# Performance work log

Measured on AMD Instinct MI355X. Metric: run time of the kernel, lower is better.

## Reference

```python
import jax, jax.numpy as jnp
import numpy as np

H = 1024          # hidden_size
V = 50257         # output_size (vocab)
L = 64            # max_length


def setup_inputs() -> dict:
    key = jax.random.key(0)
    ks = jax.random.split(key, 20)
    s = 0.02
    inp = {
        "input": jax.random.randint(ks[0], (1,), 0, V, dtype=jnp.int64) if jax.config.jax_enable_x64 else jax.random.randint(ks[0], (1,), 0, V, dtype=jnp.int32),
        "hidden": jax.random.normal(ks[1], (2, 1, H), dtype=jnp.float32),
        "encoder_output": jax.random.normal(ks[2], (1, 2 * H), dtype=jnp.float32),
        "encoder_outputs": jax.random.normal(ks[3], (L, 2 * H), dtype=jnp.float32),
        # parameters
        "emb": jax.random.normal(ks[4], (V, H), dtype=jnp.float32) * s,
        "attn_W": jax.random.normal(ks[5], (L, 3 * H), dtype=jnp.float32) * s,
        "attn_b": jnp.zeros((L,), dtype=jnp.float32),
        "comb_W": jax.random.normal(ks[6], (H, 3 * H), dtype=jnp.float32) * s,
        "comb_b": jnp.zeros((H,), dtype=jnp.float32),
        "Wih_f": jax.random.normal(ks[7], (3 * H, H), dtype=jnp.float32) * s,
        "Whh_f": jax.random.normal(ks[8], (3 * H, H), dtype=jnp.float32) * s,
        "bih_f": jnp.zeros((3 * H,), dtype=jnp.float32),
        "bhh_f": jnp.zeros((3 * H,), dtype=jnp.float32),
        "Wih_b": jax.random.normal(ks[9], (3 * H, H), dtype=jnp.float32) * s,
        "Whh_b": jax.random.normal(ks[10], (3 * H, H), dtype=jnp.float32) * s,
        "bih_b": jnp.zeros((3 * H,), dtype=jnp.float32),
        "bhh_b": jnp.zeros((3 * H,), dtype=jnp.float32),
        "out_W": jax.random.normal(ks[11], (V, 2 * H), dtype=jnp.float32) * s,
        "out_b": jnp.zeros((V,), dtype=jnp.float32),
    }
    return inp


def _gru_cell(x, h, Wih, Whh, bih, bhh):
    # PyTorch GRUCell gate math; x, h: (1, H)
    gi = x @ Wih.T + bih                      # (1, 3H)
    gh = h @ Whh.T + bhh                      # (1, 3H)
    ir, iz, inn = jnp.split(gi, 3, axis=1)
    hr, hz, hn = jnp.split(gh, 3, axis=1)
    r = jax.nn.sigmoid(ir + hr)
    z = jax.nn.sigmoid(iz + hz)
    n = jnp.tanh(inn + r * hn)
    return (1.0 - z) * n + z * h


def reference(input, hidden, encoder_output, encoder_outputs,
              emb, attn_W, attn_b, comb_W, comb_b,
              Wih_f, Whh_f, bih_f, bhh_f,
              Wih_b, Whh_b, bih_b, bhh_b,
              out_W, out_b):
    embedded = emb[input]                     # (1, H); dropout is identity in eval
    h0, h1 = hidden[0], hidden[1]             # (1, H) each
    cat3 = jnp.concatenate([embedded, h0, h1], axis=1)          # (1, 3H)
    attn_weights = jax.nn.softmax(cat3 @ attn_W.T + attn_b, axis=1)  # (1, L)
    attn_applied = attn_weights @ encoder_outputs               # (1, 2H)
    comb = jnp.concatenate([embedded, attn_applied], axis=1)    # (1, 3H)
    x = jax.nn.relu(comb @ comb_W.T + comb_b)                   # (1, H)
    hf = _gru_cell(x, h0, Wih_f, Whh_f, bih_f, bhh_f)           # forward dir
    hb = _gru_cell(x, h1, Wih_b, Whh_b, bih_b, bhh_b)           # backward dir (seq_len=1)
    gru_out = jnp.concatenate([hf, hb], axis=1)                 # (1, 2H)
    new_hidden = jnp.stack([hf, hb], axis=0)                    # (2, 1, H)
    log_probs = jax.nn.log_softmax(gru_out @ out_W.T + out_b, axis=1)  # (1, V)
    return (log_probs, new_hidden, attn_weights)
```

## Files before the change

kernel.cpp:

```cpp
#include <hip/hip_runtime.h>
#include <hip/hip_bf16.h>
#include <math.h>

#define H   1024
#define V   50257
#define L   64
#define H2  2048
#define H3  3072

#define WS_ATTN_LOGITS 0
#define WS_ATTNW       64
#define WS_AA          128
#define WS_X           2176
#define WS_GRU         3200
#define WS_LOGITS      5248
#define WS_RED         55552
#define WS_C           55680

__device__ inline float waveReduceSum(float v) {
#pragma unroll
    for (int off = 32; off > 0; off >>= 1) v += __shfl_down(v, off, 64);
    return v;
}
__device__ inline float waveAllMax(float v) {
#pragma unroll
    for (int off = 32; off > 0; off >>= 1) v = fmaxf(v, __shfl_xor(v, off, 64));
    return v;
}
__device__ inline float waveAllSum(float v) {
#pragma unroll
    for (int off = 32; off > 0; off >>= 1) v += __shfl_xor(v, off, 64);
    return v;
}

__global__ __launch_bounds__(256) void k_attn_logits(
        const int* __restrict__ tok_p, const float* __restrict__ hidden,
        const float* __restrict__ emb, const float* __restrict__ attn_W,
        const float* __restrict__ attn_b, float* __restrict__ ws) {
    int b = blockIdx.x;
    int tid = threadIdx.x;
    int tok = tok_p[0];
    const float4* w4   = (const float4*)(attn_W + (size_t)b * H3);
    const float4* emb4 = (const float4*)(emb + (size_t)tok * H);
    const float4* hid4 = (const float4*)hidden;
    float acc = 0.f;
#pragma unroll
    for (int k = 0; k < 3; ++k) {
        int idx = tid + k * 256;
        float4 c = (idx < 256) ? emb4[idx] : hid4[idx - 256];
        float4 w = w4[idx];
        acc += c.x * w.x + c.y * w.y + c.z * w.z + c.w * w.w;
    }
    __shared__ float red[4];
    float p = waveReduceSum(acc);
    int lane = tid & 63, wid = tid >> 6;
    if (lane == 0) red[wid] = p;
    __syncthreads();
    if (tid == 0) ws[WS_ATTN_LOGITS + b] = red[0] + red[1] + red[2] + red[3] + attn_b[b];
}

__global__ __launch_bounds__(64) void k_softmax64(float* __restrict__ ws,
                                                  float* __restrict__ d_out) {
    int lane = threadIdx.x;
    float x = ws[WS_ATTN_LOGITS + lane];
    float m = waveAllMax(x);
    float e = expf(x - m);
    float s = waveAllSum(e);
    float w = e / s;
    ws[WS_ATTNW + lane] = w;
    d_out[V + H2 + lane] = w;
}

__global__ __launch_bounds__(256) void k_attn_applied(
        const float* __restrict__ eo, float* __restrict__ ws) {
    int j = blockIdx.x * 256 + threadIdx.x;
    float acc = 0.f;
#pragma unroll 8
    for (int l = 0; l < L; ++l) acc += ws[WS_ATTNW + l] * eo[l * H2 + j];
    ws[WS_AA + j] = acc;
}

__global__ __launch_bounds__(256) void k_comb_relu(
        const int* __restrict__ tok_p, const float* __restrict__ emb,
        const float* __restrict__ comb_W, const float* __restrict__ comb_b,
        float* __restrict__ ws) {
    int tid = threadIdx.x;
    int lane = tid & 63, wid = tid >> 6;
    int r = blockIdx.x * 4 + wid;
    int tok = tok_p[0];
    const float4* emb4 = (const float4*)(emb + (size_t)tok * H);
    const float4* aa4  = (const float4*)(ws + WS_AA);
    const float4* w4   = (const float4*)(comb_W + (size_t)r * H3);
    float acc = 0.f;
#pragma unroll
    for (int k = 0; k < 12; ++k) {
        int idx = lane + k * 64;
        float4 c = (idx < 256) ? emb4[idx] : aa4[idx - 256];
        float4 w = w4[idx];
        acc += c.x * w.x + c.y * w.y + c.z * w.z + c.w * w.w;
    }
    acc = waveReduceSum(acc);
    if (lane == 0) ws[WS_X + r] = fmaxf(acc + comb_b[r], 0.f);
}

__global__ __launch_bounds__(256) void k_gru(
        const float* __restrict__ hidden,
        const float* __restrict__ Wih_f, const float* __restrict__ Whh_f,
        const float* __restrict__ bih_f, const float* __restrict__ bhh_f,
        const float* __restrict__ Wih_b, const float* __restrict__ Whh_b,
        const float* __restrict__ bih_b, const float* __restrict__ bhh_b,
        float* __restrict__ d_out, float* __restrict__ ws) {
    int tid = threadIdx.x;
    int lane = tid & 63, wid = tid >> 6;
    int w = blockIdx.x * 4 + wid;
    int dir = w >> 10;
    int i = w & (H - 1);
    const float* Wih = dir ? Wih_b : Wih_f;
    const float* Whh = dir ? Whh_b : Whh_f;
    const float* bih = dir ? bih_b : bih_f;
    const float* bhh = dir ? bhh_b : bhh_f;
    const float* h = hidden + dir * H;
    const float4* x4  = (const float4*)(ws + WS_X);
    const float4* h4  = (const float4*)h;
    const float4* wi0 = (const float4*)(Wih + (size_t)i * H);
    const float4* wi1 = (const float4*)(Wih + (size_t)(H + i) * H);
    const float4* wi2 = (const float4*)(Wih + (size_t)(2 * H + i) * H);
    const float4* wh0 = (const float4*)(Whh + (size_t)i * H);
    const float4* wh1 = (const float4*)(Whh + (size_t)(H + i) * H);
    const float4* wh2 = (const float4*)(Whh + (size_t)(2 * H + i) * H);
    float a0 = 0, a1 = 0, a2 = 0, b0 = 0, b1 = 0, b2 = 0;
#pragma unroll
    for (int k = 0; k < 4; ++k) {
        int idx = lane + k * 64;
        float4 xv = x4[idx], hv = h4[idx];
        float4 u0 = wi0[idx], u1 = wi1[idx], u2 = wi2[idx];
        float4 v0 = wh0[idx], v1 = wh1[idx], v2 = wh2[idx];
        a0 += xv.x*u0.x + xv.y*u0.y + xv.z*u0.z + xv.w*u0.w;
        a1 += xv.x*u1.x + xv.y*u1.y + xv.z*u1.z + xv.w*u1.w;
        a2 += xv.x*u2.x + xv.y*u2.y + xv.z*u2.z + xv.w*u2.w;
        b0 += hv.x*v0.x + hv.y*v0.y + hv.z*v0.z + hv.w*v0.w;
        b1 += hv.x*v1.x + hv.y*v1.y + hv.z*v1.z + hv.w*v1.w;
        b2 += hv.x*v2.x + hv.y*v2.y + hv.z*v2.z + hv.w*v2.w;
    }
    a0 = waveReduceSum(a0); a1 = waveReduceSum(a1); a2 = waveReduceSum(a2);
    b0 = waveReduceSum(b0); b1 = waveReduceSum(b1); b2 = waveReduceSum(b2);
    if (lane == 0) {
        float ir = a0 + bih[i],     iz = a1 + bih[H + i], in_ = a2 + bih[2 * H + i];
        float hr = b0 + bhh[i],     hz = b1 + bhh[H + i], hn  = b2 + bhh[2 * H + i];
        float r = 1.f / (1.f + expf(-(ir + hr)));
        float z = 1.f / (1.f + expf(-(iz + hz)));
        float n = tanhf(in_ + r * hn);
        float hv = (1.f - z) * n + z * h[i];
        d_out[V + dir * H + i] = hv;
        ws[WS_GRU + dir * H + i] = hv;
    }
}

__global__ __launch_bounds__(256) void k_out_gemv(
        const float* __restrict__ out_W, const float* __restrict__ out_b,
        float* __restrict__ ws) {
    int tid = threadIdx.x;
    int lane = tid & 63, wid = tid >> 6;
    int v = blockIdx.x * 4 + wid;
    if (v >= V) return;
    const float4* g4 = (const float4*)(ws + WS_GRU);
    const float4* w4 = (const float4*)(out_W + (size_t)v * H2);
    float acc = 0.f;
#pragma unroll
    for (int k = 0; k < 8; ++k) {
        int idx = lane + k * 64;
        float4 g = g4[idx], w = w4[idx];
        acc += g.x * w.x + g.y * w.y + g.z * w.z + g.w * w.w;
    }
    acc = waveReduceSum(acc);
    if (lane == 0) ws[WS_LOGITS + v] = acc + out_b[v];
}

__device__ inline void lse_combine(float& m, float& s, float m2, float s2) {
    float M = fmaxf(m, m2);
    s = s * expf(m - M) + s2 * expf(m2 - M);
    m = M;
}

__global__ __launch_bounds__(256) void k_lse_partial(float* __restrict__ ws) {
    int tid = blockIdx.x * 256 + threadIdx.x;
    int stride = gridDim.x * 256;
    float m = -3.0e38f, s = 0.f;
    for (int v = tid; v < V; v += stride) {
        float x = ws[WS_LOGITS + v];
        float M = fmaxf(m, x);
        s = s * expf(m - M) + expf(x - M);
        m = M;
    }
#pragma unroll
    for (int off = 32; off > 0; off >>= 1) {
        float m2 = __shfl_xor(m, off, 64);
        float s2 = __shfl_xor(s, off, 64);
        lse_combine(m, s, m2, s2);
    }
    __shared__ float mm[4], ss[4];
    int lane = threadIdx.x & 63, wid = threadIdx.x >> 6;
    if (lane == 0) { mm[wid] = m; ss[wid] = s; }
    __syncthreads();
    if (threadIdx.x == 0) {
        float M = mm[0], S = ss[0];
        lse_combine(M, S, mm[1], ss[1]);
        lse_combine(M, S, mm[2], ss[2]);
        lse_combine(M, S, mm[3], ss[3]);
        ws[WS_RED + 2 * blockIdx.x]     = M;
        ws[WS_RED + 2 * blockIdx.x + 1] = S;
    }
}

__global__ __launch_bounds__(64) void k_lse_final(float* __restrict__ ws) {
    int lane = threadIdx.x;
    float m = ws[WS_RED + 2 * lane];
    float s = ws[WS_RED + 2 * lane + 1];
#pragma unroll
    for (int off = 32; off > 0; off >>= 1) {
        float m2 = __shfl_xor(m, off, 64);
        float s2 = __shfl_xor(s, off, 64);
        lse_combine(m, s, m2, s2);
    }
    if (lane == 0) ws[WS_C] = m + logf(s);
}

__global__ __launch_bounds__(256) void k_sub(const float* __restrict__ ws,
                                             float* __restrict__ d_out) {
    int v = blockIdx.x * 256 + threadIdx.x;
    if (v < V) d_out[v] = ws[WS_LOGITS + v] - ws[WS_C];
}

extern "C" void kernel_launch(void* const* d_in, const int* in_sizes, int n_in,
                              void* d_out, int out_size, void* d_ws, size_t ws_size,
                              hipStream_t stream) {
    const int*   tok     = (const int*)  d_in[0];
    const float* hidden  = (const float*)d_in[1];
    const float* enc_outs= (const float*)d_in[3];
    const float* emb     = (const float*)d_in[4];
    const float* attn_W  = (const float*)d_in[5];
    const float* attn_b  = (const float*)d_in[6];
    const float* comb_W  = (const float*)d_in[7];
    const float* comb_b  = (const float*)d_in[8];
    const float* Wih_f   = (const float*)d_in[9];
    const float* Whh_f   = (const float*)d_in[10];
    const float* bih_f   = (const float*)d_in[11];
    const float* bhh_f   = (const float*)d_in[12];
    const float* Wih_b   = (const float*)d_in[13];
    const float* Whh_b   = (const float*)d_in[14];
    const float* bih_b   = (const float*)d_in[15];
    const float* bhh_b   = (const float*)d_in[16];
    const float* out_W   = (const float*)d_in[17];
    const float* out_b   = (const float*)d_in[18];
    float* out = (float*)d_out;
    float* ws  = (float*)d_ws;

    hipLaunchKernelGGL(k_attn_logits, dim3(64), dim3(256), 0, stream,
                       tok, hidden, emb, attn_W, attn_b, ws);
    hipLaunchKernelGGL(k_softmax64, dim3(1), dim3(64), 0, stream, ws, out);
    hipLaunchKernelGGL(k_attn_applied, dim3(8), dim3(256), 0, stream, enc_outs, ws);
    hipLaunchKernelGGL(k_comb_relu, dim3(256), dim3(256), 0, stream,
                       tok, emb, comb_W, comb_b, ws);
    hipLaunchKernelGGL(k_gru, dim3(512), dim3(256), 0, stream,
                       hidden, Wih_f, Whh_f, bih_f, bhh_f,
                       Wih_b, Whh_b, bih_b, bhh_b, out, ws);
    hipLaunchKernelGGL(k_out_gemv, dim3((V + 3) / 4), dim3(256), 0, stream,
                       out_W, out_b, ws);
    hipLaunchKernelGGL(k_lse_partial, dim3(64), dim3(256), 0, stream, ws);
    hipLaunchKernelGGL(k_lse_final, dim3(1), dim3(64), 0, stream, ws);
    hipLaunchKernelGGL(k_sub, dim3(197), dim3(256), 0, stream, ws, out);
}
```

Measured before the change: 105.7 us.

## Fuse front stages into cooperative kernel and fold LSE into output GEMV

The attention, softmax, attention-apply, combine and GRU stages are merged into one cooperative kernel with grid-wide syncs, replacing five launches. The vocab GEMV becomes a persistent grid-stride kernel that also computes per-block online log-sum-exp partials. The final reduction and subtraction are merged, so nine launches drop to three. Grid syncs cost something, and the cooperative launch needs all 512 blocks co-resident. Every block of the subtract kernel also redundantly re-reduces 1024 partials.

```diff
diff --git a/kernel.cpp b/kernel.cpp
--- a/kernel.cpp
+++ b/kernel.cpp
@@ -1,6 +1,9 @@
 #include <hip/hip_runtime.h>
 #include <hip/hip_bf16.h>
+#include <hip/hip_cooperative_groups.h>
 #include <math.h>
+
+namespace cg = cooperative_groups;
 
 #define H   1024
 #define V   50257
@@ -9,13 +12,14 @@
 #define H3  3072
 
 #define WS_ATTN_LOGITS 0
-#define WS_ATTNW       64
 #define WS_AA          128
 #define WS_X           2176
 #define WS_GRU         3200
 #define WS_LOGITS      5248
 #define WS_RED         55552
-#define WS_C           55680
+
+#define GEMV_BLOCKS 1024
+#define GEMV_WAVES  (GEMV_BLOCKS * 4)
 
 __device__ inline float waveReduceSum(float v) {
 #pragma unroll
@@ -32,177 +36,163 @@
     for (int off = 32; off > 0; off >>= 1) v += __shfl_xor(v, off, 64);
     return v;
 }
-
-__global__ __launch_bounds__(256) void k_attn_logits(
+__device__ inline void lse_combine(float& m, float& s, float m2, float s2) {
+    float M = fmaxf(m, m2);
+    s = s * expf(m - M) + s2 * expf(m2 - M);
+    m = M;
+}
+
+__global__ __launch_bounds__(256) void k_front(
         const int* __restrict__ tok_p, const float* __restrict__ hidden,
         const float* __restrict__ emb, const float* __restrict__ attn_W,
-        const float* __restrict__ attn_b, float* __restrict__ ws) {
-    int b = blockIdx.x;
-    int tid = threadIdx.x;
-    int tok = tok_p[0];
-    const float4* w4   = (const float4*)(attn_W + (size_t)b * H3);
-    const float4* emb4 = (const float4*)(emb + (size_t)tok * H);
-    const float4* hid4 = (const float4*)hidden;
-    float acc = 0.f;
-#pragma unroll
-    for (int k = 0; k < 3; ++k) {
-        int idx = tid + k * 256;
-        float4 c = (idx < 256) ? emb4[idx] : hid4[idx - 256];
-        float4 w = w4[idx];
-        acc += c.x * w.x + c.y * w.y + c.z * w.z + c.w * w.w;
-    }
-    __shared__ float red[4];
-    float p = waveReduceSum(acc);
-    int lane = tid & 63, wid = tid >> 6;
-    if (lane == 0) red[wid] = p;
-    __syncthreads();
-    if (tid == 0) ws[WS_ATTN_LOGITS + b] = red[0] + red[1] + red[2] + red[3] + attn_b[b];
-}
-
-__global__ __launch_bounds__(64) void k_softmax64(float* __restrict__ ws,
-                                                  float* __restrict__ d_out) {
-    int lane = threadIdx.x;
-    float x = ws[WS_ATTN_LOGITS + lane];
-    float m = waveAllMax(x);
-    float e = expf(x - m);
-    float s = waveAllSum(e);
-    float w = e / s;
-    ws[WS_ATTNW + lane] = w;
-    d_out[V + H2 + lane] = w;
-}
-
-__global__ __launch_bounds__(256) void k_attn_applied(
-        const float* __restrict__ eo, float* __restrict__ ws) {
-    int j = blockIdx.x * 256 + threadIdx.x;
-    float acc = 0.f;
-#pragma unroll 8
-    for (int l = 0; l < L; ++l) acc += ws[WS_ATTNW + l] * eo[l * H2 + j];
-    ws[WS_AA + j] = acc;
-}
-
-__global__ __launch_bounds__(256) void k_comb_relu(
-        const int* __restrict__ tok_p, const float* __restrict__ emb,
+        const float* __restrict__ attn_b, const float* __restrict__ eo,
         const float* __restrict__ comb_W, const float* __restrict__ comb_b,
-        float* __restrict__ ws) {
-    int tid = threadIdx.x;
-    int lane = tid & 63, wid = tid >> 6;
-    int r = blockIdx.x * 4 + wid;
-    int tok = tok_p[0];
-    const float4* emb4 = (const float4*)(emb + (size_t)tok * H);
-    const float4* aa4  = (const float4*)(ws + WS_AA);
-    const float4* w4   = (const float4*)(comb_W + (size_t)r * H3);
-    float acc = 0.f;
-#pragma unroll
-    for (int k = 0; k < 12; ++k) {
-        int idx = lane + k * 64;
-        float4 c = (idx < 256) ? emb4[idx] : aa4[idx - 256];
-        float4 w = w4[idx];
-        acc += c.x * w.x + c.y * w.y + c.z * w.z + c.w * w.w;
-    }
-    acc = waveReduceSum(acc);
-    if (lane == 0) ws[WS_X + r] = fmaxf(acc + comb_b[r], 0.f);
-}
-
-__global__ __launch_bounds__(256) void k_gru(
-        const float* __restrict__ hidden,
         const float* __restrict__ Wih_f, const float* __restrict__ Whh_f,
         const float* __restrict__ bih_f, const float* __restrict__ bhh_f,
         const float* __restrict__ Wih_b, const float* __restrict__ Whh_b,
         const float* __restrict__ bih_b, const float* __restrict__ bhh_b,
         float* __restrict__ d_out, float* __restrict__ ws) {
+    cg::grid_group grid = cg::this_grid();
     int tid = threadIdx.x;
     int lane = tid & 63, wid = tid >> 6;
-    int w = blockIdx.x * 4 + wid;
-    int dir = w >> 10;
-    int i = w & (H - 1);
-    const float* Wih = dir ? Wih_b : Wih_f;
-    const float* Whh = dir ? Whh_b : Whh_f;
-    const float* bih = dir ? bih_b : bih_f;
-    const float* bhh = dir ? bhh_b : bhh_f;
-    const float* h = hidden + dir * H;
-    const float4* x4  = (const float4*)(ws + WS_X);
-    const float4* h4  = (const float4*)h;
-    const float4* wi0 = (const float4*)(Wih + (size_t)i * H);
-    const float4* wi1 = (const float4*)(Wih + (size_t)(H + i) * H);
-    const float4* wi2 = (const float4*)(Wih + (size_t)(2 * H + i) * H);
-    const float4* wh0 = (const float4*)(Whh + (size_t)i * H);
-    const float4* wh1 = (const float4*)(Whh + (size_t)(H + i) * H);
-    const float4* wh2 = (const float4*)(Whh + (size_t)(2 * H + i) * H);
-    float a0 = 0, a1 = 0, a2 = 0, b0 = 0, b1 = 0, b2 = 0;
-#pragma unroll
-    for (int k = 0; k < 4; ++k) {
-        int idx = lane + k * 64;
-        float4 xv = x4[idx], hv = h4[idx];
-        float4 u0 = wi0[idx], u1 = wi1[idx], u2 = wi2[idx];
-        float4 v0 = wh0[idx], v1 = wh1[idx], v2 = wh2[idx];
-        a0 += xv.x*u0.x + xv.y*u0.y + xv.z*u0.z + xv.w*u0.w;
-        a1 += xv.x*u1.x + xv.y*u1.y + xv.z*u1.z + xv.w*u1.w;
-        a2 += xv.x*u2.x + xv.y*u2.y + xv.z*u2.z + xv.w*u2.w;
-        b0 += hv.x*v0.x + hv.y*v0.y + hv.z*v0.z + hv.w*v0.w;
-        b1 += hv.x*v1.x + hv.y*v1.y + hv.z*v1.z + hv.w*v1.w;
-        b2 += hv.x*v2.x + hv.y*v2.y + hv.z*v2.z + hv.w*v2.w;
-    }
-    a0 = waveReduceSum(a0); a1 = waveReduceSum(a1); a2 = waveReduceSum(a2);
-    b0 = waveReduceSum(b0); b1 = waveReduceSum(b1); b2 = waveReduceSum(b2);
-    if (lane == 0) {
-        float ir = a0 + bih[i],     iz = a1 + bih[H + i], in_ = a2 + bih[2 * H + i];
-        float hr = b0 + bhh[i],     hz = b1 + bhh[H + i], hn  = b2 + bhh[2 * H + i];
-        float r = 1.f / (1.f + expf(-(ir + hr)));
-        float z = 1.f / (1.f + expf(-(iz + hz)));
-        float n = tanhf(in_ + r * hn);
-        float hv = (1.f - z) * n + z * h[i];
-        d_out[V + dir * H + i] = hv;
-        ws[WS_GRU + dir * H + i] = hv;
-    }
-}
-
-__global__ __launch_bounds__(256) void k_out_gemv(
+    int bid = blockIdx.x;
+    __shared__ float red[4];
+    __shared__ float aw[64];
+
+    int tok = tok_p[0];
+    const float4* emb4 = (const float4*)(emb + (size_t)tok * H);
+    const float4* hid4 = (const float4*)hidden;
+
+    if (bid < 64) {
+        const float4* w4 = (const float4*)(attn_W + (size_t)bid * H3);
+        float acc = 0.f;
+#pragma unroll
+        for (int k = 0; k < 3; ++k) {
+            int idx = tid + k * 256;
+            float4 c = (idx < 256) ? emb4[idx] : hid4[idx - 256];
+            float4 w = w4[idx];
+            acc += c.x * w.x + c.y * w.y + c.z * w.z + c.w * w.w;
+        }
+        float p = waveReduceSum(acc);
+        if (lane == 0) red[wid] = p;
+        __syncthreads();
+        if (tid == 0)
+            ws[WS_ATTN_LOGITS + bid] = red[0] + red[1] + red[2] + red[3] + attn_b[bid];
+    }
+    grid.sync();
+
+    if (bid < 8) {
+        if (tid < 64) {
+            float x = ws[WS_ATTN_LOGITS + tid];
+            float m = waveAllMax(x);
+            float e = expf(x - m);
+            float s = waveAllSum(e);
+            float w = e / s;
+            aw[tid] = w;
+            if (bid == 0) d_out[V + H2 + tid] = w;
+        }
+        __syncthreads();
+        int j = bid * 256 + tid;
+        float acc = 0.f;
+#pragma unroll 8
+        for (int l = 0; l < L; ++l) acc += aw[l] * eo[l * H2 + j];
+        ws[WS_AA + j] = acc;
+    }
+    grid.sync();
+
+    if (bid < 256) {
+        int r = bid * 4 + wid;
+        const float4* aa4 = (const float4*)(ws + WS_AA);
+        const float4* w4  = (const float4*)(comb_W + (size_t)r * H3);
+        float acc = 0.f;
+#pragma unroll
+        for (int k = 0; k < 12; ++k) {
+            int idx = lane + k * 64;
+            float4 c = (idx < 256) ? emb4[idx] : aa4[idx - 256];
+            float4 w = w4[idx];
+            acc += c.x * w.x + c.y * w.y + c.z * w.z + c.w * w.w;
+        }
+        acc = waveReduceSum(acc);
+        if (lane == 0) ws[WS_X + r] = fmaxf(acc + comb_b[r], 0.f);
+    }
+    grid.sync();
+
+    {
+        int w = bid * 4 + wid;
+        int dir = w >> 10;
+        int i = w & (H - 1);
+        const float* Wih = dir ? Wih_b : Wih_f;
+        const float* Whh = dir ? Whh_b : Whh_f;
+        const float* bih = dir ? bih_b : bih_f;
+        const float* bhh = dir ? bhh_b : bhh_f;
+        const float* h = hidden + dir * H;
+        const float4* x4  = (const float4*)(ws + WS_X);
+        const float4* h4  = (const float4*)h;
+        const float4* wi0 = (const float4*)(Wih + (size_t)i * H);
+        const float4* wi1 = (const float4*)(Wih + (size_t)(H + i) * H);
+        const float4* wi2 = (const float4*)(Wih + (size_t)(2 * H + i) * H);
+        const float4* wh0 = (const float4*)(Whh + (size_t)i * H);
+        const float4* wh1 = (const float4*)(Whh + (size_t)(H + i) * H);
+        const float4* wh2 = (const float4*)(Whh + (size_t)(2 * H + i) * H);
+        float a0 = 0, a1 = 0, a2 = 0, b0 = 0, b1 = 0, b2 = 0;
+#pragma unroll
+        for (int k = 0; k < 4; ++k) {
+            int idx = lane + k * 64;
+            float4 xv = x4[idx], hv = h4[idx];
+            float4 u0 = wi0[idx], u1 = wi1[idx], u2 = wi2[idx];
+            float4 v0 = wh0[idx], v1 = wh1[idx], v2 = wh2[idx];
+            a0 += xv.x*u0.x + xv.y*u0.y + xv.z*u0.z + xv.w*u0.w;
+            a1 += xv.x*u1.x + xv.y*u1.y + xv.z*u1.z + xv.w*u1.w;
+            a2 += xv.x*u2.x + xv.y*u2.y + xv.z*u2.z + xv.w*u2.w;
+            b0 += hv.x*v0.x + hv.y*v0.y + hv.z*v0.z + hv.w*v0.w;
+            b1 += hv.x*v1.x + hv.y*v1.y + hv.z*v1.z + hv.w*v1.w;
+            b2 += hv.x*v2.x + hv.y*v2.y + hv.z*v2.z + hv.w*v2.w;
+        }
+        a0 = waveReduceSum(a0); a1 = waveReduceSum(a1); a2 = waveReduceSum(a2);
+        b0 = waveReduceSum(b0); b1 = waveReduceSum(b1); b2 = waveReduceSum(b2);
+        if (lane == 0) {
+            float ir = a0 + bih[i],     iz = a1 + bih[H + i], in_ = a2 + bih[2 * H + i];
+            float hr = b0 + bhh[i],     hz = b1 + bhh[H + i], hn  = b2 + bhh[2 * H + i];
+            float r = 1.f / (1.f + expf(-(ir + hr)));
+            float z = 1.f / (1.f + expf(-(iz + hz)));
+            float n = tanhf(in_ + r * hn);
+            float hv = (1.f - z) * n + z * h[i];
+            d_out[V + dir * H + i] = hv;
+            ws[WS_GRU + dir * H + i] = hv;
+        }
+    }
+}
+
+__global__ __launch_bounds__(256) void k_gemv_lse(
         const float* __restrict__ out_W, const float* __restrict__ out_b,
         float* __restrict__ ws) {
     int tid = threadIdx.x;
     int lane = tid & 63, wid = tid >> 6;
-    int v = blockIdx.x * 4 + wid;
-    if (v >= V) return;
+    int gw = blockIdx.x * 4 + wid;
     const float4* g4 = (const float4*)(ws + WS_GRU);
-    const float4* w4 = (const float4*)(out_W + (size_t)v * H2);
-    float acc = 0.f;
-#pragma unroll
-    for (int k = 0; k < 8; ++k) {
-        int idx = lane + k * 64;
-        float4 g = g4[idx], w = w4[idx];
-        acc += g.x * w.x + g.y * w.y + g.z * w.z + g.w * w.w;
-    }
-    acc = waveReduceSum(acc);
-    if (lane == 0) ws[WS_LOGITS + v] = acc + out_b[v];
-}
-
-__device__ inline void lse_combine(float& m, float& s, float m2, float s2) {
-    float M = fmaxf(m, m2);
-    s = s * expf(m - M) + s2 * expf(m2 - M);
-    m = M;
-}
-
-__global__ __launch_bounds__(256) void k_lse_partial(float* __restrict__ ws) {
-    int tid = blockIdx.x * 256 + threadIdx.x;
-    int stride = gridDim.x * 256;
     float m = -3.0e38f, s = 0.f;
-    for (int v = tid; v < V; v += stride) {
-        float x = ws[WS_LOGITS + v];
-        float M = fmaxf(m, x);
-        s = s * expf(m - M) + expf(x - M);
-        m = M;
-    }
-#pragma unroll
-    for (int off = 32; off > 0; off >>= 1) {
-        float m2 = __shfl_xor(m, off, 64);
-        float s2 = __shfl_xor(s, off, 64);
-        lse_combine(m, s, m2, s2);
+    for (int v = gw; v < V; v += GEMV_WAVES) {
+        const float4* w4 = (const float4*)(out_W + (size_t)v * H2);
+        float acc = 0.f;
+#pragma unroll
+        for (int k = 0; k < 8; ++k) {
+            int idx = lane + k * 64;
+            float4 g = g4[idx], w = w4[idx];
+            acc += g.x * w.x + g.y * w.y + g.z * w.z + g.w * w.w;
+        }
+        acc = waveReduceSum(acc);
+        if (lane == 0) {
+            float logit = acc + out_b[v];
+            ws[WS_LOGITS + v] = logit;
+            float M = fmaxf(m, logit);
+            s = s * expf(m - M) + expf(logit - M);
+            m = M;
+        }
     }
     __shared__ float mm[4], ss[4];
-    int lane = threadIdx.x & 63, wid = threadIdx.x >> 6;
     if (lane == 0) { mm[wid] = m; ss[wid] = s; }
     __syncthreads();
-    if (threadIdx.x == 0) {
+    if (tid == 0) {
         float M = mm[0], S = ss[0];
         lse_combine(M, S, mm[1], ss[1]);
         lse_combine(M, S, mm[2], ss[2]);
@@ -212,23 +202,36 @@
     }
 }
 
-__global__ __launch_bounds__(64) void k_lse_final(float* __restrict__ ws) {
-    int lane = threadIdx.x;
-    float m = ws[WS_RED + 2 * lane];
-    float s = ws[WS_RED + 2 * lane + 1];
+__global__ __launch_bounds__(256) void k_lse_sub(const float* __restrict__ ws,
+                                                 float* __restrict__ d_out) {
+    int tid = threadIdx.x;
+    int lane = tid & 63, wid = tid >> 6;
+    float m = -3.0e38f, s = 0.f;
+#pragma unroll
+    for (int k = 0; k < 4; ++k) {
+        int i = tid + k * 256;
+        lse_combine(m, s, ws[WS_RED + 2 * i], ws[WS_RED + 2 * i + 1]);
+    }
 #pragma unroll
     for (int off = 32; off > 0; off >>= 1) {
         float m2 = __shfl_xor(m, off, 64);
         float s2 = __shfl_xor(s, off, 64);
         lse_combine(m, s, m2, s2);
     }
-    if (lane == 0) ws[WS_C] = m + logf(s);
-}
-
-__global__ __launch_bounds__(256) void k_sub(const float* __restrict__ ws,
-                                             float* __restrict__ d_out) {
-    int v = blockIdx.x * 256 + threadIdx.x;
-    if (v < V) d_out[v] = ws[WS_LOGITS + v] - ws[WS_C];
+    __shared__ float mm[4], ss[4], Csh;
+    if (lane == 0) { mm[wid] = m; ss[wid] = s; }
+    __syncthreads();
+    if (tid == 0) {
+        float M = mm[0], S = ss[0];
+        lse_combine(M, S, mm[1], ss[1]);
+        lse_combine(M, S, mm[2], ss[2]);
+        lse_combine(M, S, mm[3], ss[3]);
+        Csh = M + logf(S);
+    }
+    __syncthreads();
+    float C = Csh;
+    int v = blockIdx.x * 256 + tid;
+    if (v < V) d_out[v] = ws[WS_LOGITS + v] - C;
 }
 
 extern "C" void kernel_launch(void* const* d_in, const int* in_sizes, int n_in,
@@ -255,18 +258,16 @@
     float* out = (float*)d_out;
     float* ws  = (float*)d_ws;
 
-    hipLaunchKernelGGL(k_attn_logits, dim3(64), dim3(256), 0, stream,
-                       tok, hidden, emb, attn_W, attn_b, ws);
-    hipLaunchKernelGGL(k_softmax64, dim3(1), dim3(64), 0, stream, ws, out);
-    hipLaunchKernelGGL(k_attn_applied, dim3(8), dim3(256), 0, stream, enc_outs, ws);
-    hipLaunchKernelGGL(k_comb_relu, dim3(256), dim3(256), 0, stream,
-                       tok, emb, comb_W, comb_b, ws);
-    hipLaunchKernelGGL(k_gru, dim3(512), dim3(256), 0, stream,
-                       hidden, Wih_f, Whh_f, bih_f, bhh_f,
-                       Wih_b, Whh_b, bih_b, bhh_b, out, ws);
-    hipLaunchKernelGGL(k_out_gemv, dim3((V + 3) / 4), dim3(256), 0, stream,
+    void* kargs[] = {
+        (void*)&tok, (void*)&hidden, (void*)&emb, (void*)&attn_W, (void*)&attn_b,
+        (void*)&enc_outs, (void*)&comb_W, (void*)&comb_b,
+        (void*)&Wih_f, (void*)&Whh_f, (void*)&bih_f, (void*)&bhh_f,
+        (void*)&Wih_b, (void*)&Whh_b, (void*)&bih_b, (void*)&bhh_b,
+        (void*)&out, (void*)&ws
+    };
+    hipLaunchCooperativeKernel((const void*)k_front, dim3(512), dim3(256),
+                               kargs, 0, stream);
+    hipLaunchKernelGGL(k_gemv_lse, dim3(GEMV_BLOCKS), dim3(256), 0, stream,
                        out_W, out_b, ws);
-    hipLaunchKernelGGL(k_lse_partial, dim3(64), dim3(256), 0, stream, ws);
-    hipLaunchKernelGGL(k_lse_final, dim3(1), dim3(64), 0, stream, ws);
-    hipLaunchKernelGGL(k_sub, dim3(197), dim3(256), 0, stream, ws, out);
-}
+    hipLaunchKernelGGL(k_lse_sub, dim3(197), dim3(256), 0, stream, ws, out);
+}
```

Measured after the change: 285.4 us. 170% more time.
